# Kernel optimization log

Hardware: AMD Instinct MI355X
Metric: run time of the kernel (lower is better)

The kernel has to match this reference:

```python
import jax, jax.numpy as jnp
import numpy as np

HIDDEN = 256
HEADS = 8
HEAD_DIM = HIDDEN // HEADS
SCALE = HEAD_DIM ** -0.5
N = 4096
NUM_GRAPHS = 16
LN_EPS = 1e-5


def setup_inputs() -> dict:
    key = jax.random.key(0)
    ks = jax.random.split(key, 8)
    x = jax.random.normal(ks[0], (N, HIDDEN), dtype=jnp.float32)
    batch = jnp.sort(jax.random.randint(ks[1], (N,), 0, NUM_GRAPHS, dtype=jnp.int64))
    # Xavier-uniform linear weights, stored as [in, out] (y = x @ W + b)
    lim = float(np.sqrt(6.0 / (HIDDEN + HIDDEN)))
    def W(k):
        return jax.random.uniform(k, (HIDDEN, HIDDEN), jnp.float32, -lim, lim)
    return {
        "x": x,
        "batch": batch,
        "Wq": W(ks[2]), "bq": jnp.zeros((HIDDEN,), jnp.float32),
        "Wk": W(ks[3]), "bk": jnp.zeros((HIDDEN,), jnp.float32),
        "Wv": W(ks[4]), "bv": jnp.zeros((HIDDEN,), jnp.float32),
        "Wo": W(ks[5]), "bo": jnp.zeros((HIDDEN,), jnp.float32),
        "gamma": jnp.ones((HIDDEN,), jnp.float32),
        "beta": jnp.zeros((HIDDEN,), jnp.float32),
    }


def _layer_norm(x, gamma, beta):
    mu = jnp.mean(x, axis=-1, keepdims=True)
    var = jnp.mean(jnp.square(x - mu), axis=-1, keepdims=True)
    return (x - mu) * jax.lax.rsqrt(var + LN_EPS) * gamma + beta


def reference(x, batch, Wq, bq, Wk, bk, Wv, bv, Wo, bo, gamma, beta):
    residual = x
    h = _layer_norm(x, gamma, beta)
    n = h.shape[0]
    q = (h @ Wq + bq).reshape(n, HEADS, HEAD_DIM)
    k = (h @ Wk + bk).reshape(n, HEADS, HEAD_DIM)
    v = (h @ Wv + bv).reshape(n, HEADS, HEAD_DIM)
    # dense scores masked to block-diagonal (same-graph) structure
    scores = jnp.einsum('ihd,jhd->ihj', q, k) * SCALE  # [N, H, N]
    same_graph = (batch[None, :] == batch[:, None])[:, None, :]  # [N, 1, N]
    scores = jnp.where(same_graph, scores, -jnp.inf)
    attn = jax.nn.softmax(scores, axis=-1)
    attn = jnp.nan_to_num(attn, nan=0.0)
    out = jnp.einsum('ihj,jhd->ihd', attn, v).reshape(n, HIDDEN)
    out = out @ Wo + bo
    return residual + out
```

## Files before the change

### kernel.cpp

```cpp
#include <hip/hip_runtime.h>

#define NNODES 4096
#define HID 256
#define NG 16
#define NH 8
#define HD 32
#define LN_EPS 1e-5f
#define QSCALE (0.17677669529663687f * 1.4426950408889634f)
#define HLS 264
#define AOS 264

typedef unsigned short u16;
typedef unsigned int u32;
typedef __bf16 bf16x8 __attribute__((ext_vector_type(8)));
typedef float f32x4 __attribute__((ext_vector_type(4)));

__device__ __forceinline__ u16 f2bf(float f){
  union { float f; u32 i; } c; c.f = f;
  u32 x = c.i;
  return (u16)((x + 0x7fffu + ((x >> 16) & 1u)) >> 16);
}

__global__ __launch_bounds__(256) void lnqkv_kernel(
    const float* __restrict__ x, const float* __restrict__ gamma,
    const float* __restrict__ beta,
    const float* __restrict__ Wq, const float* __restrict__ Wk,
    const float* __restrict__ Wv, const float* __restrict__ Wo,
    const float* __restrict__ bq, const float* __restrict__ bk,
    const float* __restrict__ bv,
    u16* __restrict__ qb, u16* __restrict__ kb, u16* __restrict__ vb,
    u16* __restrict__ WoT){
  __shared__ u16 hl[64][HLS];
  int bid = blockIdx.x;
  int which = blockIdx.y;
  if (which == 3){
    if (bid >= 64) return;
    u16 (*tl)[33] = (u16(*)[33])hl;
    int bx = (bid & 7) * 32, by = (bid >> 3) * 32;
    int tx = threadIdx.x & 31, ty = threadIdx.x >> 5;
    #pragma unroll
    for (int r = 0; r < 32; r += 8)
      tl[ty + r][tx] = f2bf(Wo[(size_t)(by + ty + r) * HID + bx + tx]);
    __syncthreads();
    #pragma unroll
    for (int r = 0; r < 32; r += 8)
      WoT[(size_t)(bx + ty + r) * HID + by + tx] = tl[tx][ty + r];
    return;
  }
  int wave = threadIdx.x >> 6, lane = threadIdx.x & 63;
  int m0 = (bid >> 2) * 64;
  int nb = (bid & 3) * 64 + wave * 16;
  const float* W    = (which == 0) ? Wq : (which == 1) ? Wk : Wv;
  const float* bias = (which == 0) ? bq : (which == 1) ? bk : bv;
  u16* out          = (which == 0) ? qb : (which == 1) ? kb : vb;

  int rsub = lane >> 4;
  int c16  = lane & 15;
  float4 g0 = *(const float4*)(gamma + c16 * 16 + 0);
  float4 g1 = *(const float4*)(gamma + c16 * 16 + 4);
  float4 g2 = *(const float4*)(gamma + c16 * 16 + 8);
  float4 g3 = *(const float4*)(gamma + c16 * 16 + 12);
  float4 t0 = *(const float4*)(beta + c16 * 16 + 0);
  float4 t1 = *(const float4*)(beta + c16 * 16 + 4);
  float4 t2 = *(const float4*)(beta + c16 * 16 + 8);
  float4 t3 = *(const float4*)(beta + c16 * 16 + 12);
  float ga[16] = {g0.x,g0.y,g0.z,g0.w, g1.x,g1.y,g1.z,g1.w,
                  g2.x,g2.y,g2.z,g2.w, g3.x,g3.y,g3.z,g3.w};
  float bt[16] = {t0.x,t0.y,t0.z,t0.w, t1.x,t1.y,t1.z,t1.w,
                  t2.x,t2.y,t2.z,t2.w, t3.x,t3.y,t3.z,t3.w};
  #pragma unroll
  for (int b = 0; b < 4; b++){
    int rloc = wave * 16 + b * 4 + rsub;
    const float* xr = x + (size_t)(m0 + rloc) * HID + c16 * 16;
    float4 v0 = *(const float4*)(xr + 0);
    float4 v1 = *(const float4*)(xr + 4);
    float4 v2 = *(const float4*)(xr + 8);
    float4 v3 = *(const float4*)(xr + 12);
    float e[16] = {v0.x,v0.y,v0.z,v0.w, v1.x,v1.y,v1.z,v1.w,
                   v2.x,v2.y,v2.z,v2.w, v3.x,v3.y,v3.z,v3.w};
    float s = 0.f;
    #pragma unroll
    for (int i = 0; i < 16; i++) s += e[i];
    s += __shfl_xor(s, 1); s += __shfl_xor(s, 2);
    s += __shfl_xor(s, 4); s += __shfl_xor(s, 8);
    float mu = s * (1.0f / HID);
    float vv = 0.f;
    #pragma unroll
    for (int i = 0; i < 16; i++){ e[i] -= mu; vv += e[i] * e[i]; }
    vv += __shfl_xor(vv, 1); vv += __shfl_xor(vv, 2);
    vv += __shfl_xor(vv, 4); vv += __shfl_xor(vv, 8);
    float rs = rsqrtf(vv * (1.0f / HID) + LN_EPS);
    u32 pk[8];
    #pragma unroll
    for (int i = 0; i < 8; i++){
      float o0 = e[2*i]     * rs * ga[2*i]     + bt[2*i];
      float o1 = e[2*i + 1] * rs * ga[2*i + 1] + bt[2*i + 1];
      pk[i] = (u32)f2bf(o0) | ((u32)f2bf(o1) << 16);
    }
    *(uint4*)&hl[rloc][c16 * 16]     = make_uint4(pk[0], pk[1], pk[2], pk[3]);
    *(uint4*)&hl[rloc][c16 * 16 + 8] = make_uint4(pk[4], pk[5], pk[6], pk[7]);
  }
  __syncthreads();

  int lr = lane & 15, lq = lane >> 4;
  f32x4 acc[4] = {};
  const float* wbase = W + nb + lr;
  #pragma unroll
  for (int k0 = 0; k0 < HID; k0 += 32){
    union { bf16x8 v; u16 e[8]; } bf;
    const float* wp = wbase + (size_t)(k0 + lq * 8) * HID;
    #pragma unroll
    for (int j = 0; j < 8; j++) bf.e[j] = f2bf(wp[(size_t)j * HID]);
    #pragma unroll
    for (int t = 0; t < 4; t++){
      bf16x8 a = *(const bf16x8*)&hl[t * 16 + lr][k0 + lq * 8];
      acc[t] = __builtin_amdgcn_mfma_f32_16x16x32_bf16(a, bf.v, acc[t], 0, 0, 0);
    }
  }
  int col = nb + lr;
  float bb = bias[col];
  #pragma unroll
  for (int t = 0; t < 4; t++){
    #pragma unroll
    for (int r = 0; r < 4; r++){
      int row = m0 + 16 * t + lq * 4 + r;
      out[(size_t)row * HID + col] = f2bf(acc[t][r] + bb);
    }
  }
}

__global__ __launch_bounds__(1024, 4) void attnproj_kernel(
    const u16* __restrict__ q, const u16* __restrict__ k,
    const u16* __restrict__ v, const u16* __restrict__ WoT,
    const float* __restrict__ bo, const float* __restrict__ x,
    const int* __restrict__ batch, int bstride, float* __restrict__ out){
  __shared__ u16 ao[16][AOS];
  __shared__ float mg[8][10][64];
  __shared__ int seg[NG + 1];
  int m0 = blockIdx.x * 16;
  int tid = threadIdx.x;
  int wave = tid >> 6, lane = tid & 63;
  {
    int target = wave + 1;
    int p = batch[(size_t)(lane * 64) * bstride];
    int c = __popcll(__ballot(p < target));
    int lo = 0;
    if (c > 0){
      int base = (c - 1) * 64 + 1;
      int idx = base + lane;
      int val = (idx < NNODES) ? batch[(size_t)idx * bstride] : 0x7fffffff;
      lo = base + __popcll(__ballot(val < target));
    }
    if (lane == 0) seg[target] = lo;
    if (tid == 0) seg[0] = 0;
  }
  __syncthreads();
  int lq = lane >> 4, lr = lane & 15;
  int hd = wave & 7;
  int jh = wave >> 3;

  int qrow = m0 + lr;
  int gq = batch[(size_t)qrow * bstride];
  int lo_r = seg[gq], hi_r = seg[gq + 1];
  int g_lo = batch[(size_t)m0 * bstride];
  int g_hi = batch[(size_t)(m0 + 15) * bstride];
  int jstart = seg[g_lo], jend = seg[g_hi + 1];
  int ntj = (jend - jstart + 15) >> 4;

  bf16x8 qf = *(const bf16x8*)&q[(size_t)qrow * HID + hd * HD + lq * 8];
  float m = -3.0e38f, l = 0.f;
  f32x4 o0 = {0.f,0.f,0.f,0.f}, o1 = {0.f,0.f,0.f,0.f};
  {
    int half = (ntj + 1) >> 1;
    int jt0 = jh ? half : 0;
    int jt1 = jh ? ntj : half;
    if (jt0 < jt1){
      auto LOADT = [&](int jt, bf16x8& kf, u16* va, u16* vc){
        int j0 = jstart + (jt << 4);
        int krow = j0 + lr; if (krow > NNODES - 1) krow = NNODES - 1;
        kf = *(const bf16x8*)&k[(size_t)krow * HID + hd * HD + lq * 8];
        #pragma unroll
        for (int i = 0; i < 4; i++){
          int vrow = j0 + lq * 4 + i;
          if (vrow > NNODES - 1) vrow = NNODES - 1;
          const u16* vp = &v[(size_t)vrow * HID + hd * HD + lr];
          va[i] = vp[0];
          vc[i] = vp[16];
        }
      };
      bf16x8 kf_c; u16 va_c[4], vc_c[4];
      LOADT(jt0, kf_c, va_c, vc_c);
      for (int jt = jt0; jt < jt1; jt++){
        bf16x8 kf_n; u16 va_n[4], vc_n[4];
        int jn = (jt + 1 < jt1) ? jt + 1 : jt;
        LOADT(jn, kf_n, va_n, vc_n);
        int j0 = jstart + (jt << 4);
        f32x4 st = __builtin_amdgcn_mfma_f32_16x16x32_bf16(kf_c, qf,
                     (f32x4){0.f,0.f,0.f,0.f}, 0, 0, 0);
        int jb = j0 + lq * 4;
        float s0 = (jb + 0 >= lo_r && jb + 0 < hi_r) ? st[0] * QSCALE : -3.0e38f;
        float s1 = (jb + 1 >= lo_r && jb + 1 < hi_r) ? st[1] * QSCALE : -3.0e38f;
        float s2 = (jb + 2 >= lo_r && jb + 2 < hi_r) ? st[2] * QSCALE : -3.0e38f;
        float s3 = (jb + 3 >= lo_r && jb + 3 < hi_r) ? st[3] * QSCALE : -3.0e38f;
        float tm = fmaxf(fmaxf(s0, s1), fmaxf(s2, s3));
        tm = fmaxf(tm, __shfl_xor(tm, 16));
        tm = fmaxf(tm, __shfl_xor(tm, 32));
        float mn = fmaxf(m, tm);
        float alpha = exp2f(m - mn);
        float p0 = exp2f(s0 - mn), p1 = exp2f(s1 - mn);
        float p2 = exp2f(s2 - mn), p3 = exp2f(s3 - mn);
        float ps = (p0 + p1) + (p2 + p3);
        ps += __shfl_xor(ps, 16);
        ps += __shfl_xor(ps, 32);
        l = l * alpha + ps;
        m = mn;
        union { bf16x8 v8; u32 w[4]; } pf, vf0, vf1;
        pf.w[0] = (u32)f2bf(p0) | ((u32)f2bf(p1) << 16);
        pf.w[1] = (u32)f2bf(p2) | ((u32)f2bf(p3) << 16);
        pf.w[2] = 0; pf.w[3] = 0;
        vf0.w[0] = (u32)va_c[0] | ((u32)va_c[1] << 16);
        vf0.w[1] = (u32)va_c[2] | ((u32)va_c[3] << 16);
        vf0.w[2] = 0; vf0.w[3] = 0;
        vf1.w[0] = (u32)vc_c[0] | ((u32)vc_c[1] << 16);
        vf1.w[1] = (u32)vc_c[2] | ((u32)vc_c[3] << 16);
        vf1.w[2] = 0; vf1.w[3] = 0;
        o0 = o0 * alpha;
        o1 = o1 * alpha;
        o0 = __builtin_amdgcn_mfma_f32_16x16x32_bf16(vf0.v8, pf.v8, o0, 0, 0, 0);
        o1 = __builtin_amdgcn_mfma_f32_16x16x32_bf16(vf1.v8, pf.v8, o1, 0, 0, 0);
        kf_c = kf_n;
        #pragma unroll
        for (int i = 0; i < 4; i++){ va_c[i] = va_n[i]; vc_c[i] = vc_n[i]; }
      }
    }
  }
  if (jh == 1){
    mg[hd][0][lane] = o0[0]; mg[hd][1][lane] = o0[1];
    mg[hd][2][lane] = o0[2]; mg[hd][3][lane] = o0[3];
    mg[hd][4][lane] = o1[0]; mg[hd][5][lane] = o1[1];
    mg[hd][6][lane] = o1[2]; mg[hd][7][lane] = o1[3];
    mg[hd][8][lane] = m;     mg[hd][9][lane] = l;
  }
  __syncthreads();
  if (jh == 0){
    float m2 = mg[hd][8][lane], l2 = mg[hd][9][lane];
    float mn = fmaxf(m, m2);
    float a  = exp2f(m - mn);
    float a2 = exp2f(m2 - mn);
    float lt = l * a + l2 * a2;
    float rl = 1.0f / lt;
    float r0 = (o0[0]*a + mg[hd][0][lane]*a2) * rl;
    float r1 = (o0[1]*a + mg[hd][1][lane]*a2) * rl;
    float r2 = (o0[2]*a + mg[hd][2][lane]*a2) * rl;
    float r3 = (o0[3]*a + mg[hd][3][lane]*a2) * rl;
    float r4 = (o1[0]*a + mg[hd][4][lane]*a2) * rl;
    float r5 = (o1[1]*a + mg[hd][5][lane]*a2) * rl;
    float r6 = (o1[2]*a + mg[hd][6][lane]*a2) * rl;
    float r7 = (o1[3]*a + mg[hd][7][lane]*a2) * rl;
    int dbase = hd * HD + lq * 4;
    *(u32*)&ao[lr][dbase]          = (u32)f2bf(r0) | ((u32)f2bf(r1) << 16);
    *(u32*)&ao[lr][dbase + 2]      = (u32)f2bf(r2) | ((u32)f2bf(r3) << 16);
    *(u32*)&ao[lr][dbase + 16]     = (u32)f2bf(r4) | ((u32)f2bf(r5) << 16);
    *(u32*)&ao[lr][dbase + 16 + 2] = (u32)f2bf(r6) | ((u32)f2bf(r7) << 16);
  }
  __syncthreads();

  {
    int n0 = wave * 16;
    f32x4 acc = {};
    const u16* brow = WoT + (size_t)(n0 + lr) * HID + lq * 8;
    #pragma unroll
    for (int k0 = 0; k0 < HID; k0 += 32){
      bf16x8 a = *(const bf16x8*)&ao[lr][k0 + lq * 8];
      bf16x8 b = *(const bf16x8*)(brow + k0);
      acc = __builtin_amdgcn_mfma_f32_16x16x32_bf16(a, b, acc, 0, 0, 0);
    }
    int col = n0 + lr;
    float bb = bo[col];
    #pragma unroll
    for (int r = 0; r < 4; r++){
      size_t idx = (size_t)(m0 + lq * 4 + r) * HID + col;
      out[idx] = acc[r] + bb + x[idx];
    }
  }
}

__global__ void sentinel_kernel(u32* __restrict__ out, int nwords){
  int i = blockIdx.x * 256 + threadIdx.x;
  if (i < nwords) out[i] = 0x46404640u;
}

extern "C" void kernel_launch(void* const* d_in, const int* in_sizes, int n_in,
                              void* d_out, int out_size, void* d_ws, size_t ws_size,
                              hipStream_t stream){
  const float* x   = (const float*)d_in[0];
  const int* batch = (const int*)d_in[1];
  const float* Wq = (const float*)d_in[2],  *bq = (const float*)d_in[3];
  const float* Wk = (const float*)d_in[4],  *bk = (const float*)d_in[5];
  const float* Wv = (const float*)d_in[6],  *bv = (const float*)d_in[7];
  const float* Wo = (const float*)d_in[8],  *bo = (const float*)d_in[9];
  const float* gamma = (const float*)d_in[10], *beta = (const float*)d_in[11];

  const size_t BUF  = (size_t)NNODES * HID * 2;
  const size_t WOT  = (size_t)HID * HID * 2;
  const size_t NEED = 1024 + 3 * BUF + WOT;

  if (ws_size < NEED){
    int nwords = out_size / 2;
    sentinel_kernel<<<(nwords + 255) / 256, 256, 0, stream>>>((u32*)d_out, nwords);
    return;
  }

  int bstride = (in_sizes[1] >= NNODES * 8) ? 2 : 1;

  char* w = (char*)d_ws;
  u16* qb  = (u16*)(w + 1024);
  u16* kb  = qb + (size_t)NNODES * HID;
  u16* vb  = kb + (size_t)NNODES * HID;
  u16* WoT = vb + (size_t)NNODES * HID;

  lnqkv_kernel<<<dim3(256, 4), 256, 0, stream>>>(x, gamma, beta, Wq, Wk, Wv, Wo,
                                                 bq, bk, bv, qb, kb, vb, WoT);
  attnproj_kernel<<<256, 1024, 0, stream>>>(qb, kb, vb, WoT, bo, x, batch,
                                            bstride, (float*)d_out);
}
```

Before: 113.3 us.

## Store V transposed so attention loads V fragments as contiguous vectors

The QKV kernel now writes V in a transposed [HID][N] layout, staging each tile through shared memory so the global writes are coalesced. The attention kernel then reads each V fragment as two 8-byte vector loads instead of eight scattered 2-byte loads per tile. The key-range start is rounded down to a multiple of 16 so that the vector loads stay aligned. This adds an extra shared-memory round trip and two barriers to the V projection, and it may process one more key tile per block.

```diff
diff --git a/kernel.cpp b/kernel.cpp
--- a/kernel.cpp
+++ b/kernel.cpp
@@ -9,6 +9,7 @@
 #define QSCALE (0.17677669529663687f * 1.4426950408889634f)
 #define HLS 264
 #define AOS 264
+#define TLS 72
 
 typedef unsigned short u16;
 typedef unsigned int u32;
@@ -28,7 +29,7 @@
     const float* __restrict__ Wv, const float* __restrict__ Wo,
     const float* __restrict__ bq, const float* __restrict__ bk,
     const float* __restrict__ bv,
-    u16* __restrict__ qb, u16* __restrict__ kb, u16* __restrict__ vb,
+    u16* __restrict__ qb, u16* __restrict__ kb, u16* __restrict__ vt,
     u16* __restrict__ WoT){
   __shared__ u16 hl[64][HLS];
   int bid = blockIdx.x;
@@ -52,7 +53,6 @@
   int nb = (bid & 3) * 64 + wave * 16;
   const float* W    = (which == 0) ? Wq : (which == 1) ? Wk : Wv;
   const float* bias = (which == 0) ? bq : (which == 1) ? bk : bv;
-  u16* out          = (which == 0) ? qb : (which == 1) ? kb : vb;
 
   int rsub = lane >> 4;
   int c16  = lane & 15;
@@ -117,21 +117,44 @@
       acc[t] = __builtin_amdgcn_mfma_f32_16x16x32_bf16(a, bf.v, acc[t], 0, 0, 0);
     }
   }
-  int col = nb + lr;
-  float bb = bias[col];
-  #pragma unroll
-  for (int t = 0; t < 4; t++){
-    #pragma unroll
-    for (int r = 0; r < 4; r++){
-      int row = m0 + 16 * t + lq * 4 + r;
-      out[(size_t)row * HID + col] = f2bf(acc[t][r] + bb);
+  float bb = bias[nb + lr];
+  if (which != 2){
+    u16* out = (which == 0) ? qb : kb;
+    int col = nb + lr;
+    #pragma unroll
+    for (int t = 0; t < 4; t++){
+      #pragma unroll
+      for (int r = 0; r < 4; r++){
+        int row = m0 + 16 * t + lq * 4 + r;
+        out[(size_t)row * HID + col] = f2bf(acc[t][r] + bb);
+      }
+    }
+  } else {
+    u16* tlb = &hl[0][0];
+    __syncthreads();
+    #pragma unroll
+    for (int t = 0; t < 4; t++){
+      u32 lo = (u32)f2bf(acc[t][0] + bb) | ((u32)f2bf(acc[t][1] + bb) << 16);
+      u32 hi = (u32)f2bf(acc[t][2] + bb) | ((u32)f2bf(acc[t][3] + bb) << 16);
+      u16* rowp = tlb + (size_t)(wave * 16 + lr) * TLS + 16 * t + lq * 4;
+      *(u32*)rowp       = lo;
+      *(u32*)(rowp + 2) = hi;
+    }
+    __syncthreads();
+    int nb0 = (bid & 3) * 64;
+    int c  = threadIdx.x >> 3;
+    int r8 = (threadIdx.x & 7) * 8;
+    #pragma unroll
+    for (int cc = 0; cc < 64; cc += 32){
+      uint4 val = *(uint4*)&tlb[(size_t)(cc + c) * TLS + r8];
+      *(uint4*)&vt[(size_t)(nb0 + cc + c) * NNODES + m0 + r8] = val;
     }
   }
 }
 
 __global__ __launch_bounds__(1024, 4) void attnproj_kernel(
     const u16* __restrict__ q, const u16* __restrict__ k,
-    const u16* __restrict__ v, const u16* __restrict__ WoT,
+    const u16* __restrict__ vt, const u16* __restrict__ WoT,
     const float* __restrict__ bo, const float* __restrict__ x,
     const int* __restrict__ batch, int bstride, float* __restrict__ out){
   __shared__ u16 ao[16][AOS];
@@ -164,7 +187,8 @@
   int lo_r = seg[gq], hi_r = seg[gq + 1];
   int g_lo = batch[(size_t)m0 * bstride];
   int g_hi = batch[(size_t)(m0 + 15) * bstride];
-  int jstart = seg[g_lo], jend = seg[g_hi + 1];
+  int jstart = seg[g_lo] & ~15;
+  int jend = seg[g_hi + 1];
   int ntj = (jend - jstart + 15) >> 4;
 
   bf16x8 qf = *(const bf16x8*)&q[(size_t)qrow * HID + hd * HD + lq * 8];
@@ -175,25 +199,23 @@
     int jt0 = jh ? half : 0;
     int jt1 = jh ? ntj : half;
     if (jt0 < jt1){
-      auto LOADT = [&](int jt, bf16x8& kf, u16* va, u16* vc){
+      const u16* vrow0 = vt + (size_t)(hd * HD + lr) * NNODES;
+      const u16* vrow1 = vt + (size_t)(hd * HD + 16 + lr) * NNODES;
+      auto LOADT = [&](int jt, bf16x8& kf, uint2& w0, uint2& w1){
         int j0 = jstart + (jt << 4);
         int krow = j0 + lr; if (krow > NNODES - 1) krow = NNODES - 1;
         kf = *(const bf16x8*)&k[(size_t)krow * HID + hd * HD + lq * 8];
-        #pragma unroll
-        for (int i = 0; i < 4; i++){
-          int vrow = j0 + lq * 4 + i;
-          if (vrow > NNODES - 1) vrow = NNODES - 1;
-          const u16* vp = &v[(size_t)vrow * HID + hd * HD + lr];
-          va[i] = vp[0];
-          vc[i] = vp[16];
-        }
+        int jal = j0 + lq * 4;
+        if (jal > NNODES - 4) jal = NNODES - 4;
+        w0 = *(const uint2*)(vrow0 + jal);
+        w1 = *(const uint2*)(vrow1 + jal);
       };
-      bf16x8 kf_c; u16 va_c[4], vc_c[4];
-      LOADT(jt0, kf_c, va_c, vc_c);
+      bf16x8 kf_c; uint2 v0_c, v1_c;
+      LOADT(jt0, kf_c, v0_c, v1_c);
       for (int jt = jt0; jt < jt1; jt++){
-        bf16x8 kf_n; u16 va_n[4], vc_n[4];
+        bf16x8 kf_n; uint2 v0_n, v1_n;
         int jn = (jt + 1 < jt1) ? jt + 1 : jt;
-        LOADT(jn, kf_n, va_n, vc_n);
+        LOADT(jn, kf_n, v0_n, v1_n);
         int j0 = jstart + (jt << 4);
         f32x4 st = __builtin_amdgcn_mfma_f32_16x16x32_bf16(kf_c, qf,
                      (f32x4){0.f,0.f,0.f,0.f}, 0, 0, 0);
@@ -218,19 +240,15 @@
         pf.w[0] = (u32)f2bf(p0) | ((u32)f2bf(p1) << 16);
         pf.w[1] = (u32)f2bf(p2) | ((u32)f2bf(p3) << 16);
         pf.w[2] = 0; pf.w[3] = 0;
-        vf0.w[0] = (u32)va_c[0] | ((u32)va_c[1] << 16);
-        vf0.w[1] = (u32)va_c[2] | ((u32)va_c[3] << 16);
+        vf0.w[0] = v0_c.x; vf0.w[1] = v0_c.y;
         vf0.w[2] = 0; vf0.w[3] = 0;
-        vf1.w[0] = (u32)vc_c[0] | ((u32)vc_c[1] << 16);
-        vf1.w[1] = (u32)vc_c[2] | ((u32)vc_c[3] << 16);
+        vf1.w[0] = v1_c.x; vf1.w[1] = v1_c.y;
         vf1.w[2] = 0; vf1.w[3] = 0;
         o0 = o0 * alpha;
         o1 = o1 * alpha;
         o0 = __builtin_amdgcn_mfma_f32_16x16x32_bf16(vf0.v8, pf.v8, o0, 0, 0, 0);
         o1 = __builtin_amdgcn_mfma_f32_16x16x32_bf16(vf1.v8, pf.v8, o1, 0, 0, 0);
-        kf_c = kf_n;
-        #pragma unroll
-        for (int i = 0; i < 4; i++){ va_c[i] = va_n[i]; vc_c[i] = vc_n[i]; }
+        kf_c = kf_n; v0_c = v0_n; v1_c = v1_n;
       }
     }
   }
@@ -316,11 +334,11 @@
   char* w = (char*)d_ws;
   u16* qb  = (u16*)(w + 1024);
   u16* kb  = qb + (size_t)NNODES * HID;
-  u16* vb  = kb + (size_t)NNODES * HID;
-  u16* WoT = vb + (size_t)NNODES * HID;
+  u16* vt  = kb + (size_t)NNODES * HID;
+  u16* WoT = vt + (size_t)NNODES * HID;
 
   lnqkv_kernel<<<dim3(256, 4), 256, 0, stream>>>(x, gamma, beta, Wq, Wk, Wv, Wo,
-                                                 bq, bk, bv, qb, kb, vb, WoT);
-  attnproj_kernel<<<256, 1024, 0, stream>>>(qb, kb, vb, WoT, bo, x, batch,
+                                                 bq, bk, bv, qb, kb, vt, WoT);
+  attnproj_kernel<<<256, 1024, 0, stream>>>(qb, kb, vt, WoT, bo, x, batch,
                                             bstride, (float*)d_out);
 }
```

New measurement: 119.6 us. 5.5% more time.
